# Optimization experiments

Measured on AMD Instinct MI355X. Metric: run time of the kernel, lower is better.

## Reference

```python
import jax, jax.numpy as jnp
import numpy as np

HEAD_LENGTH = 4  # hardcoded in original source; scale = 1/sqrt(4) = 0.5
SCALE = 1.0 / HEAD_LENGTH ** 0.5
MASK_FILL = -1.0e9

B, H, S, D = 2, 12, 2048, 64


def setup_inputs() -> dict:
    key = jax.random.key(0)
    kq, kk, kv, km = jax.random.split(key, 4)
    q = jax.random.normal(kq, (B, H, S, D), dtype=jnp.float32)
    k = jax.random.normal(kk, (B, H, S, D), dtype=jnp.float32)
    v = jax.random.normal(kv, (B, H, S, D), dtype=jnp.float32)
    mask = jax.random.randint(km, (B, H, S, S), 0, 2).astype(jnp.bool_)
    return {"q": q, "k": k, "v": v, "mask": mask}


def reference(q, k, v, mask):
    # scores: [B, H, S, S]
    scores = jnp.einsum("bhqd,bhkd->bhqk", q, k) * SCALE
    scores = jnp.where(mask, MASK_FILL, scores)
    attn = jax.nn.softmax(scores, axis=-1)
    # dropout is identity in eval/deterministic mode
    context = jnp.einsum("bhqk,bhkd->bhqd", attn, v)
    return (context, attn)
```

## Files before the change

kernel.cpp:

```cpp
#include <hip/hip_runtime.h>
#include <cstdint>
#include <math.h>

#define S 2048
#define D 64
#define NH 24
#define CTX_ELEMS ((size_t)NH * S * D)
#define SDP_SCALE 0.5f
#define MASK_FILL -1.0e9f

#define PQW 260
#define VQW 76

typedef __attribute__((ext_vector_type(8))) short   bf16x8;
typedef __attribute__((ext_vector_type(4))) float   f32x4;
typedef __attribute__((ext_vector_type(4))) unsigned short us4;

__device__ __forceinline__ unsigned short f2bf(float x) {
    unsigned u = __builtin_bit_cast(unsigned, x);
    u += 0x7FFFu + ((u >> 16) & 1u);
    return (unsigned short)(u >> 16);
}
__device__ __forceinline__ float bf2f(unsigned short b) {
    unsigned u = ((unsigned)b) << 16;
    return __builtin_bit_cast(float, u);
}

__global__ __launch_bounds__(1024, 4) void sdpa_fused(
    const float* __restrict__ q, const float* __restrict__ k,
    const float* __restrict__ v, const int* __restrict__ mask,
    float* __restrict__ out)
{
    const int t    = threadIdx.x;
    const int w    = t >> 6;
    const int lane = t & 63;
    const int quad = lane >> 4, n = lane & 15;
    const int rbase = blockIdx.x * 16;
    const int bh    = rbase >> 11;

    __shared__ __align__(16) char pool[16640 + 38912];
    unsigned char* maskS = (unsigned char*)pool;
    float*          pq   = (float*)pool;
    unsigned short* vq   = (unsigned short*)(pool + 16640);

    __shared__ float mwS[16][16];
    __shared__ float lwS[16][16];
    __shared__ float MS[16];
    __shared__ float iLS[16];
    __shared__ float ctxred[16 * D];

    ctxred[t] = 0.f;

    {
        const int4* m4p = (const int4*)(mask + (size_t)rbase * S);
        #pragma unroll
        for (int u = 0; u < 8; ++u) {
            const int idx = u * 1024 + t;
            int4 mv = m4p[idx];
            uchar4 mb;
            mb.x = (unsigned char)(mv.x != 0);
            mb.y = (unsigned char)(mv.y != 0);
            mb.z = (unsigned char)(mv.z != 0);
            mb.w = (unsigned char)(mv.w != 0);
            *(uchar4*)&maskS[idx * 4] = mb;
        }
    }

    bf16x8 qfh[2], qfl[2];
    #pragma unroll
    for (int ks = 0; ks < 2; ++ks) {
        const float* qp = q + (size_t)(rbase + n) * D + ks * 32 + quad * 8;
        float4 a = *(const float4*)qp;
        float4 b = *(const float4*)(qp + 4);
        float c[8] = {a.x, a.y, a.z, a.w, b.x, b.y, b.z, b.w};
        #pragma unroll
        for (int u = 0; u < 8; ++u) {
            unsigned short hb = f2bf(c[u]);
            qfh[ks][u] = (short)hb;
            qfl[ks][u] = (short)f2bf(c[u] - bf2f(hb));
        }
    }
    __syncthreads();

    const float* khead = k + (size_t)bh * S * D;
    const float* vhead = v + (size_t)bh * S * D;

    float s_reg[8][4];
    float m4[4] = {-INFINITY, -INFINITY, -INFINITY, -INFINITY};
    #pragma unroll
    for (int i = 0; i < 8; ++i) {
        const int tile = w + 16 * i;
        f32x4 c = {0.f, 0.f, 0.f, 0.f};
        #pragma unroll
        for (int ks = 0; ks < 2; ++ks) {
            const float* kp = khead + (size_t)(tile * 16 + n) * D + ks * 32 + quad * 8;
            float4 ka = *(const float4*)kp;
            float4 kb = *(const float4*)(kp + 4);
            float ce[8] = {ka.x, ka.y, ka.z, ka.w, kb.x, kb.y, kb.z, kb.w};
            bf16x8 bh_, bl_;
            #pragma unroll
            for (int u = 0; u < 8; ++u) {
                unsigned short hb = f2bf(ce[u]);
                bh_[u] = (short)hb;
                bl_[u] = (short)f2bf(ce[u] - bf2f(hb));
            }
            c = __builtin_amdgcn_mfma_f32_16x16x32_bf16(qfh[ks], bh_, c, 0, 0, 0);
            c = __builtin_amdgcn_mfma_f32_16x16x32_bf16(qfl[ks], bh_, c, 0, 0, 0);
            c = __builtin_amdgcn_mfma_f32_16x16x32_bf16(qfh[ks], bl_, c, 0, 0, 0);
        }
        #pragma unroll
        for (int r = 0; r < 4; ++r) {
            float sv = c[r] * SDP_SCALE;
            if (maskS[(quad * 4 + r) * 2048 + tile * 16 + n]) sv = MASK_FILL;
            s_reg[i][r] = sv;
            m4[r] = fmaxf(m4[r], sv);
        }
    }

    #pragma unroll
    for (int r = 0; r < 4; ++r) {
        #pragma unroll
        for (int off = 1; off < 16; off <<= 1)
            m4[r] = fmaxf(m4[r], __shfl_xor(m4[r], off, 64));
    }
    float l4[4] = {0.f, 0.f, 0.f, 0.f};
    #pragma unroll
    for (int i = 0; i < 8; ++i) {
        #pragma unroll
        for (int r = 0; r < 4; ++r) {
            float e = __expf(s_reg[i][r] - m4[r]);
            s_reg[i][r] = e;
            l4[r] += e;
        }
    }
    #pragma unroll
    for (int r = 0; r < 4; ++r) {
        #pragma unroll
        for (int off = 1; off < 16; off <<= 1)
            l4[r] += __shfl_xor(l4[r], off, 64);
    }
    if (n == 0) {
        #pragma unroll
        for (int r = 0; r < 4; ++r) {
            mwS[w][quad * 4 + r] = m4[r];
            lwS[w][quad * 4 + r] = l4[r];
        }
    }
    __syncthreads();

    if (t < 16) {
        float M = -INFINITY;
        #pragma unroll
        for (int ww = 0; ww < 16; ++ww) M = fmaxf(M, mwS[ww][t]);
        float L = 0.f;
        #pragma unroll
        for (int ww = 0; ww < 16; ++ww) L += lwS[ww][t] * __expf(mwS[ww][t] - M);
        MS[t]  = M;
        iLS[t] = 1.0f / L;
    }
    __syncthreads();

    float f4[4];
    #pragma unroll
    for (int r = 0; r < 4; ++r)
        f4[r] = __expf(m4[r] - MS[quad * 4 + r]) * iLS[quad * 4 + r];

    float* attn = out + CTX_ELEMS;
    const int s_sl = w & 7;
    const int dt0  = (w >> 3) * 2;
    f32x4 acc2[2] = {{0.f,0.f,0.f,0.f},{0.f,0.f,0.f,0.f}};

    #pragma unroll
    for (int ch = 0; ch < 8; ++ch) {
        {
            const float4* v4 = (const float4*)(vhead + (size_t)ch * 256 * D);
            #pragma unroll
            for (int u = 0; u < 4; ++u) {
                const int idx = u * 1024 + t;
                const int kloc = idx >> 4, d0 = (idx & 15) * 4;
                float4 vv = v4[idx];
                us4 vb = { f2bf(vv.x), f2bf(vv.y), f2bf(vv.z), f2bf(vv.w) };
                *(us4*)&vq[kloc * VQW + d0] = vb;
            }
        }
        #pragma unroll
        for (int r = 0; r < 4; ++r)
            pq[(quad * 4 + r) * PQW + w * 16 + n] = s_reg[ch][r] * f4[r];
        __syncthreads();

        {
            const int row = t >> 6, c4 = (t & 63) * 4;
            float4 pv = *(const float4*)&pq[row * PQW + c4];
            *(float4*)(attn + (size_t)(rbase + row) * S + ch * 256 + c4) = pv;
        }

        bf16x8 af;
        {
            const float* ap = &pq[n * PQW + s_sl * 32 + quad * 8];
            float4 a0 = *(const float4*)ap;
            float4 a1 = *(const float4*)(ap + 4);
            af[0] = (short)f2bf(a0.x); af[1] = (short)f2bf(a0.y);
            af[2] = (short)f2bf(a0.z); af[3] = (short)f2bf(a0.w);
            af[4] = (short)f2bf(a1.x); af[5] = (short)f2bf(a1.y);
            af[6] = (short)f2bf(a1.z); af[7] = (short)f2bf(a1.w);
        }
        #pragma unroll
        for (int di = 0; di < 2; ++di) {
            const int dt = dt0 + di;
            bf16x8 vb;
            #pragma unroll
            for (int j = 0; j < 8; ++j)
                vb[j] = (short)vq[(s_sl * 32 + quad * 8 + j) * VQW + dt * 16 + n];
            acc2[di] = __builtin_amdgcn_mfma_f32_16x16x32_bf16(af, vb, acc2[di], 0, 0, 0);
        }
        __syncthreads();
    }

    #pragma unroll
    for (int di = 0; di < 2; ++di) {
        #pragma unroll
        for (int r = 0; r < 4; ++r)
            atomicAdd(&ctxred[(quad * 4 + r) * D + (dt0 + di) * 16 + n], acc2[di][r]);
    }
    __syncthreads();

    out[(size_t)(rbase + (t >> 6)) * D + (t & 63)] = ctxred[t];
}

extern "C" void kernel_launch(void* const* d_in, const int* in_sizes, int n_in,
                              void* d_out, int out_size, void* d_ws, size_t ws_size,
                              hipStream_t stream) {
    const float* q    = (const float*)d_in[0];
    const float* k    = (const float*)d_in[1];
    const float* v    = (const float*)d_in[2];
    const int*   mask = (const int*)d_in[3];
    float* out = (float*)d_out;

    sdpa_fused<<<NH * S / 16, 1024, 0, stream>>>(q, k, v, mask, out);
}
```

Measured before the change: 1.137 ms.

## Precompute bf16 K/V MFMA fragments in a preprocess kernel and double-buffer P

Adds a preprocessing kernel that splits K into hi/lo bf16 pairs and converts V to bf16, writing both to workspace already arranged in MFMA fragment order. The main kernel then loads K and V fragments directly from global memory, dropping the per-block redundant fp32 loads and conversions (each K/V head was reconverted by 128 blocks) and the V staging in shared memory. The P tile is double-buffered so each chunk needs one barrier instead of two. In exchange there is an extra launch and a workspace round trip, and V fragment reads in the preprocess kernel are strided.

```diff
diff --git a/kernel.cpp b/kernel.cpp
--- a/kernel.cpp
+++ b/kernel.cpp
@@ -8,13 +8,12 @@
 #define CTX_ELEMS ((size_t)NH * S * D)
 #define SDP_SCALE 0.5f
 #define MASK_FILL -1.0e9f
-
 #define PQW 260
-#define VQW 76
-
-typedef __attribute__((ext_vector_type(8))) short   bf16x8;
-typedef __attribute__((ext_vector_type(4))) float   f32x4;
-typedef __attribute__((ext_vector_type(4))) unsigned short us4;
+#define KE  ((size_t)NH * S * D)
+
+typedef __attribute__((ext_vector_type(8))) short          bf16x8;
+typedef __attribute__((ext_vector_type(4))) float          f32x4;
+typedef __attribute__((ext_vector_type(8))) unsigned short us8;
 
 __device__ __forceinline__ unsigned short f2bf(float x) {
     unsigned u = __builtin_bit_cast(unsigned, x);
@@ -26,10 +25,54 @@
     return __builtin_bit_cast(float, u);
 }
 
+__global__ __launch_bounds__(256) void sdpa_preproc(
+    const float* __restrict__ k, const float* __restrict__ v,
+    unsigned short* __restrict__ ws)
+{
+    const int g = blockIdx.x * 256 + threadIdx.x;
+    unsigned short* khi = ws;
+    unsigned short* klo = ws + KE;
+    unsigned short* vfr = ws + 2 * KE;
+
+    if (g < 393216) {
+        const int lane = g & 63, n = lane & 15, quad = lane >> 4;
+        const int ks   = (g >> 6) & 1;
+        const int tile = (g >> 7) & 127;
+        const int bh   = g >> 14;
+        const float* kp = k + (size_t)bh * S * D + (size_t)(tile * 16 + n) * D
+                            + ks * 32 + quad * 8;
+        float4 a = *(const float4*)kp;
+        float4 b = *(const float4*)(kp + 4);
+        float c[8] = {a.x, a.y, a.z, a.w, b.x, b.y, b.z, b.w};
+        us8 h, l;
+        #pragma unroll
+        for (int u = 0; u < 8; ++u) {
+            unsigned short hb = f2bf(c[u]);
+            h[u] = hb;
+            l[u] = f2bf(c[u] - bf2f(hb));
+        }
+        *(us8*)(khi + (size_t)g * 8) = h;
+        *(us8*)(klo + (size_t)g * 8) = l;
+    } else {
+        const int g2 = g - 393216;
+        const int lane = g2 & 63, n = lane & 15, quad = lane >> 4;
+        const int dt = (g2 >> 6) & 3;
+        const int sl = (g2 >> 8) & 7;
+        const int ch = (g2 >> 11) & 7;
+        const int bh = g2 >> 14;
+        const float* vp = v + (size_t)bh * S * D
+                            + (size_t)(ch * 256 + sl * 32 + quad * 8) * D
+                            + dt * 16 + n;
+        us8 o;
+        #pragma unroll
+        for (int j = 0; j < 8; ++j) o[j] = f2bf(vp[(size_t)j * D]);
+        *(us8*)(vfr + (size_t)g2 * 8) = o;
+    }
+}
+
 __global__ __launch_bounds__(1024, 4) void sdpa_fused(
-    const float* __restrict__ q, const float* __restrict__ k,
-    const float* __restrict__ v, const int* __restrict__ mask,
-    float* __restrict__ out)
+    const float* __restrict__ q, const int* __restrict__ mask,
+    const unsigned short* __restrict__ ws, float* __restrict__ out)
 {
     const int t    = threadIdx.x;
     const int w    = t >> 6;
@@ -38,10 +81,13 @@
     const int rbase = blockIdx.x * 16;
     const int bh    = rbase >> 11;
 
-    __shared__ __align__(16) char pool[16640 + 38912];
+    const unsigned short* khi = ws;
+    const unsigned short* klo = ws + KE;
+    const unsigned short* vfr = ws + 2 * KE;
+
+    __shared__ __align__(16) char pool[2 * 16 * PQW * 4];
     unsigned char* maskS = (unsigned char*)pool;
-    float*          pq   = (float*)pool;
-    unsigned short* vq   = (unsigned short*)(pool + 16640);
+    float*         pq    = (float*)pool;
 
     __shared__ float mwS[16][16];
     __shared__ float lwS[16][16];
@@ -82,32 +128,23 @@
     }
     __syncthreads();
 
-    const float* khead = k + (size_t)bh * S * D;
-    const float* vhead = v + (size_t)bh * S * D;
-
     float s_reg[8][4];
     float m4[4] = {-INFINITY, -INFINITY, -INFINITY, -INFINITY};
     #pragma unroll
     for (int i = 0; i < 8; ++i) {
         const int tile = w + 16 * i;
+        const size_t kb = ((((size_t)bh * 128 + tile) * 2) * 64 + lane) * 8;
+        bf16x8 kh0 = *(const bf16x8*)(khi + kb);
+        bf16x8 kl0 = *(const bf16x8*)(klo + kb);
+        bf16x8 kh1 = *(const bf16x8*)(khi + kb + 512);
+        bf16x8 kl1 = *(const bf16x8*)(klo + kb + 512);
         f32x4 c = {0.f, 0.f, 0.f, 0.f};
-        #pragma unroll
-        for (int ks = 0; ks < 2; ++ks) {
-            const float* kp = khead + (size_t)(tile * 16 + n) * D + ks * 32 + quad * 8;
-            float4 ka = *(const float4*)kp;
-            float4 kb = *(const float4*)(kp + 4);
-            float ce[8] = {ka.x, ka.y, ka.z, ka.w, kb.x, kb.y, kb.z, kb.w};
-            bf16x8 bh_, bl_;
-            #pragma unroll
-            for (int u = 0; u < 8; ++u) {
-                unsigned short hb = f2bf(ce[u]);
-                bh_[u] = (short)hb;
-                bl_[u] = (short)f2bf(ce[u] - bf2f(hb));
-            }
-            c = __builtin_amdgcn_mfma_f32_16x16x32_bf16(qfh[ks], bh_, c, 0, 0, 0);
-            c = __builtin_amdgcn_mfma_f32_16x16x32_bf16(qfl[ks], bh_, c, 0, 0, 0);
-            c = __builtin_amdgcn_mfma_f32_16x16x32_bf16(qfh[ks], bl_, c, 0, 0, 0);
-        }
+        c = __builtin_amdgcn_mfma_f32_16x16x32_bf16(qfh[0], kh0, c, 0, 0, 0);
+        c = __builtin_amdgcn_mfma_f32_16x16x32_bf16(qfl[0], kh0, c, 0, 0, 0);
+        c = __builtin_amdgcn_mfma_f32_16x16x32_bf16(qfh[0], kl0, c, 0, 0, 0);
+        c = __builtin_amdgcn_mfma_f32_16x16x32_bf16(qfh[1], kh1, c, 0, 0, 0);
+        c = __builtin_amdgcn_mfma_f32_16x16x32_bf16(qfl[1], kh1, c, 0, 0, 0);
+        c = __builtin_amdgcn_mfma_f32_16x16x32_bf16(qfh[1], kl1, c, 0, 0, 0);
         #pragma unroll
         for (int r = 0; r < 4; ++r) {
             float sv = c[r] * SDP_SCALE;
@@ -171,32 +208,23 @@
     f32x4 acc2[2] = {{0.f,0.f,0.f,0.f},{0.f,0.f,0.f,0.f}};
 
     #pragma unroll
+    for (int r = 0; r < 4; ++r)
+        pq[(quad * 4 + r) * PQW + w * 16 + n] = s_reg[0][r] * f4[r];
+
+    #pragma unroll
     for (int ch = 0; ch < 8; ++ch) {
-        {
-            const float4* v4 = (const float4*)(vhead + (size_t)ch * 256 * D);
-            #pragma unroll
-            for (int u = 0; u < 4; ++u) {
-                const int idx = u * 1024 + t;
-                const int kloc = idx >> 4, d0 = (idx & 15) * 4;
-                float4 vv = v4[idx];
-                us4 vb = { f2bf(vv.x), f2bf(vv.y), f2bf(vv.z), f2bf(vv.w) };
-                *(us4*)&vq[kloc * VQW + d0] = vb;
-            }
-        }
-        #pragma unroll
-        for (int r = 0; r < 4; ++r)
-            pq[(quad * 4 + r) * PQW + w * 16 + n] = s_reg[ch][r] * f4[r];
         __syncthreads();
+        float* pb = pq + (ch & 1) * 16 * PQW;
 
         {
             const int row = t >> 6, c4 = (t & 63) * 4;
-            float4 pv = *(const float4*)&pq[row * PQW + c4];
+            float4 pv = *(const float4*)&pb[row * PQW + c4];
             *(float4*)(attn + (size_t)(rbase + row) * S + ch * 256 + c4) = pv;
         }
 
         bf16x8 af;
         {
-            const float* ap = &pq[n * PQW + s_sl * 32 + quad * 8];
+            const float* ap = &pb[n * PQW + s_sl * 32 + quad * 8];
             float4 a0 = *(const float4*)ap;
             float4 a1 = *(const float4*)(ap + 4);
             af[0] = (short)f2bf(a0.x); af[1] = (short)f2bf(a0.y);
@@ -204,17 +232,23 @@
             af[4] = (short)f2bf(a1.x); af[5] = (short)f2bf(a1.y);
             af[6] = (short)f2bf(a1.z); af[7] = (short)f2bf(a1.w);
         }
+
         #pragma unroll
         for (int di = 0; di < 2; ++di) {
-            const int dt = dt0 + di;
-            bf16x8 vb;
+            const size_t vb_off =
+                (((((size_t)bh * 8 + ch) * 8 + s_sl) * 4 + (dt0 + di)) * 64 + lane) * 8;
+            bf16x8 vb = *(const bf16x8*)(vfr + vb_off);
+            acc2[di] = __builtin_amdgcn_mfma_f32_16x16x32_bf16(af, vb, acc2[di], 0, 0, 0);
+        }
+
+        if (ch < 7) {
+            float* pn = pq + ((ch + 1) & 1) * 16 * PQW;
             #pragma unroll
-            for (int j = 0; j < 8; ++j)
-                vb[j] = (short)vq[(s_sl * 32 + quad * 8 + j) * VQW + dt * 16 + n];
-            acc2[di] = __builtin_amdgcn_mfma_f32_16x16x32_bf16(af, vb, acc2[di], 0, 0, 0);
-        }
-        __syncthreads();
-    }
+            for (int r = 0; r < 4; ++r)
+                pn[(quad * 4 + r) * PQW + w * 16 + n] = s_reg[ch + 1][r] * f4[r];
+        }
+    }
+    __syncthreads();
 
     #pragma unroll
     for (int di = 0; di < 2; ++di) {
@@ -235,6 +269,8 @@
     const float* v    = (const float*)d_in[2];
     const int*   mask = (const int*)d_in[3];
     float* out = (float*)d_out;
-
-    sdpa_fused<<<NH * S / 16, 1024, 0, stream>>>(q, k, v, mask, out);
-}
+    unsigned short* ws = (unsigned short*)d_ws;
+
+    sdpa_preproc<<<3072, 256, 0, stream>>>(k, v, ws);
+    sdpa_fused<<<NH * S / 16, 1024, 0, stream>>>(q, mask, ws, out);
+}
```

Result: faster. 939.1 us (-17.4%).
